# Kernel tuning notes

Hardware: AMD Instinct MI355X
Metric: run time of the kernel (lower is better)

The kernel has to match this reference:

```python
import jax, jax.numpy as jnp
import numpy as np

B, T, V, E, DC, H = 128, 25, 10000, 512, 512, 512
N0 = H + E + DC  # layer-0 concat width
N1 = 2 * H       # layer-1 concat width


def setup_inputs() -> dict:
    key = jax.random.key(0)
    ks = jax.random.split(key, 12)
    def w(k, n):
        return jax.random.normal(k, (n, H), dtype=jnp.float32) / np.float32(np.sqrt(n))
    return {
        "tokens": jax.random.randint(ks[0], (B, T), 0, V),
        "processed_cnn_features": jax.random.normal(ks[1], (B, DC), dtype=jnp.float32),
        "initial_hidden_state": jnp.zeros((2, B, H), dtype=jnp.float32),
        "embedding": jax.random.normal(ks[2], (V, E), dtype=jnp.float32) * 0.1,
        "Wu0": w(ks[3], N0), "Wr0": w(ks[4], N0), "Wc0": w(ks[5], N0),
        "bu0": jnp.zeros((H,), jnp.float32), "br0": jnp.zeros((H,), jnp.float32), "bc0": jnp.zeros((H,), jnp.float32),
        "Wu1": w(ks[6], N1), "Wr1": w(ks[7], N1), "Wc1": w(ks[8], N1),
        "bu1": jnp.zeros((H,), jnp.float32), "br1": jnp.zeros((H,), jnp.float32), "bc1": jnp.zeros((H,), jnp.float32),
        "Wout": jax.random.normal(ks[9], (H, V), dtype=jnp.float32) / np.float32(np.sqrt(H)),
        "bout": jnp.zeros((V,), jnp.float32),
    }


def gru_step(x, h, Wu, bu, Wr, br, Wc, bc):
    xh = jnp.concatenate([x, h], axis=1)
    u = jax.nn.sigmoid(xh @ Wu + bu)
    r = jax.nn.sigmoid(xh @ Wr + br)
    cand = jnp.tanh(jnp.concatenate([x, r * h], axis=1) @ Wc + bc)
    return u * h + (1.0 - u) * cand


def reference(tokens, processed_cnn_features, initial_hidden_state, embedding,
              Wu0, Wr0, Wc0, bu0, br0, bc0,
              Wu1, Wr1, Wc1, bu1, br1, bc1,
              Wout, bout):
    emb = embedding[tokens]              # [B, T, E]
    emb_t = jnp.transpose(emb, (1, 0, 2))  # [T, B, E]

    def step(carry, e_t):
        h0, h1 = carry
        x0 = jnp.concatenate([e_t, processed_cnn_features], axis=1)  # [B, E+DC]
        h0 = gru_step(x0, h0, Wu0, bu0, Wr0, br0, Wc0, bc0)
        h1 = gru_step(h0, h1, Wu1, bu1, Wr1, br1, Wc1, bc1)
        logits = h1 @ Wout + bout  # [B, V]
        return (h0, h1), logits

    (h0, h1), logits_seq = jax.lax.scan(step, (initial_hidden_state[0], initial_hidden_state[1]), emb_t)
    logits = jnp.transpose(logits_seq, (1, 0, 2))  # [B, T, V]
    final_hidden = jnp.stack([h0, h1])             # [2, B, H]
    return logits, final_hidden
```

## Files before the change

### kernel.cpp

```cpp
#include <hip/hip_runtime.h>

#define T_ 25
#define V_ 10000
#define NWG_ 192
#define NGRP_ 8
#define GSZ_ (NWG_ / NGRP_)

typedef short bf16x8 __attribute__((ext_vector_type(8)));
typedef float f32x4 __attribute__((ext_vector_type(4)));

__device__ __forceinline__ short f2bf(float x) {
  union { float f; unsigned u; } v; v.f = x;
  unsigned r = (v.u + 0x7fffu + ((v.u >> 16) & 1u)) >> 16;
  return (short)r;
}
__device__ __forceinline__ float sigm(float z) { return 1.f / (1.f + __expf(-z)); }
__device__ __forceinline__ float tanhfast(float z) {
  float e = __expf(2.f * z);
  return 1.f - 2.f / (e + 1.f);
}

__device__ __forceinline__ void gload_lds16(const void* g, void* l) {
  __builtin_amdgcn_global_load_lds((const __attribute__((address_space(1))) void*)g,
                                   (__attribute__((address_space(3))) void*)l, 16, 0, 0);
}

__device__ __forceinline__ void vwait0() { asm volatile("s_waitcnt vmcnt(0)" ::: "memory"); }
__device__ __forceinline__ void cload16(bf16x8* d, const short* p) {
  asm volatile("global_load_dwordx4 %0, %1, off sc0 sc1" : "=v"(*d) : "v"(p) : "memory");
}
__device__ __forceinline__ void cloadf(float* d, const float* p) {
  asm volatile("global_load_dword %0, %1, off sc0 sc1" : "=v"(*d) : "v"(p) : "memory");
}
__device__ __forceinline__ void cstoref(float* p, float v) {
  asm volatile("global_store_dword %0, %1, off sc0 sc1" :: "v"(p), "v"(v) : "memory");
}
__device__ __forceinline__ void cstores(short* p, int v) {
  asm volatile("global_store_short %0, %1, off sc0 sc1" :: "v"(p), "v"(v) : "memory");
}

__device__ __forceinline__ int FL(int row, int col) {
  return (((col >> 5) * 8 + (row >> 4)) << 9) | (((row & 15) | (((col >> 3) & 3) << 4)) << 3) | (col & 7);
}

__device__ __forceinline__ void gbar(int* bar, int gen) {
  vwait0();
  __syncthreads();
  if (threadIdx.x == 0) {
    const int g = blockIdx.x & (NGRP_ - 1);
    int prev = __hip_atomic_fetch_add(&bar[256 + g * 32], 1, __ATOMIC_RELAXED, __HIP_MEMORY_SCOPE_AGENT);
    if (prev == gen * GSZ_ - 1) {
      int sp = __hip_atomic_fetch_add(&bar[512], 1, __ATOMIC_RELAXED, __HIP_MEMORY_SCOPE_AGENT);
      if (sp == gen * NGRP_ - 1) {
#pragma unroll
        for (int i = 0; i < NGRP_; i++)
          __hip_atomic_store(&bar[i * 32], gen, __ATOMIC_RELAXED, __HIP_MEMORY_SCOPE_AGENT);
      }
    }
    while (__hip_atomic_load(&bar[g * 32], __ATOMIC_RELAXED, __HIP_MEMORY_SCOPE_AGENT) < gen)
      __builtin_amdgcn_s_sleep(1);
  }
  __syncthreads();
}

struct TJob { const float* src; short* dst; int R, C, t0; };
struct TJobs { TJob j[10]; };

__global__ void tcast_all(TJobs J) {
  __shared__ float t[32][33];
  int bid = blockIdx.x;
  int ji = 0;
  while (ji < 9 && bid >= J.j[ji + 1].t0) ji++;
  const float* src = J.j[ji].src;
  short* dst = J.j[ji].dst;
  int R = J.j[ji].R, C = J.j[ji].C;
  int rel = bid - J.j[ji].t0;
  int ctiles = (C + 31) >> 5;
  int rt0 = (rel / ctiles) * 32, ct0 = (rel % ctiles) * 32;
  int tx = threadIdx.x, ty = threadIdx.y;
#pragma unroll
  for (int i = 0; i < 4; i++) {
    int r = rt0 + ty + i * 8, c = ct0 + tx;
    if (r < R && c < C) t[ty + i * 8][tx] = src[(size_t)r * C + c];
  }
  __syncthreads();
#pragma unroll
  for (int i = 0; i < 4; i++) {
    int c = ct0 + ty + i * 8, r = rt0 + tx;
    if (r < R && c < C) dst[(size_t)c * R + r] = f2bf(t[tx][ty + i * 8]);
  }
}

__global__ void build_x0(const int* __restrict__ tok, const float* __restrict__ emb,
                         const float* __restrict__ cnn, short* __restrict__ X0) {
  int row = blockIdx.x;
  int t = row >> 7, b = row & 127;
  int tk = tok[b * T_ + t];
  const float* er = emb + (size_t)tk * 512;
  short* dst = X0 + (size_t)row * 1024;
  for (int i = threadIdx.x; i < 1024; i += 256)
    dst[i] = f2bf(i < 512 ? er[i] : cnn[b * 512 + (i - 512)]);
}

__global__ void init_h(const float* __restrict__ ihs, float* h0f, float* h1f, short* xh1b) {
  int i = blockIdx.x * 256 + threadIdx.x;
  if (i < 65536) {
    int b = i >> 9, h = i & 511;
    float v0 = ihs[i], v1 = ihs[65536 + i];
    h0f[i] = v0; h1f[i] = v1;
    xh1b[FL(b, h)] = f2bf(v0);
    xh1b[FL(b, 512 + h)] = f2bf(v1);
  }
}

__global__ void write_final(const float* __restrict__ h0f, const float* __restrict__ h1f,
                            float* __restrict__ out) {
  int i = blockIdx.x * 256 + threadIdx.x;
  if (i < 65536) {
    out[32000000 + i] = h0f[i];
    out[32000000 + 65536 + i] = h1f[i];
  }
}

struct RP {
  short *xh1b, *rh0b, *xc1b0, *xc1b1, *H1all;
  float *u0f, *u1f, *h0f, *h1f;
  const float *A0;
  const short *Whur0T, *Whc0T, *W1urT, *Wc1T;
  const float *bu1, *br1, *bc1;
  int *bar;
};

template<int NKS>
__device__ __forceinline__ void wload(const short* __restrict__ Wt, int n0, int lane, bf16x8* wfr) {
  const short* p = Wt + (size_t)(n0 + (lane & 15)) * (NKS * 32) + ((lane >> 4) * 8);
#pragma unroll
  for (int ks = 0; ks < NKS; ks++) wfr[ks] = *(const bf16x8*)(p + (size_t)ks * 32);
}

template<int NKS>
__device__ __forceinline__ void kcompute_coh(const short* __restrict__ A, int rb0, int lane,
                                             const bf16x8* __restrict__ wfr, f32x4* acc) {
  const short* ap = A + rb0 * 512 + lane * 8;
  constexpr int NCH = NKS / 4;
  bf16x8 s0[2][4], s1[2][4];
#pragma unroll
  for (int j = 0; j < 4; j++) {
    cload16(&s0[0][j], ap + j * 4096);
    cload16(&s1[0][j], ap + j * 4096 + 512);
  }
#pragma unroll
  for (int c = 0; c < NCH; c++) {
    const int cb = c & 1;
    if (c + 1 < NCH) {
#pragma unroll
      for (int j = 0; j < 4; j++) {
        int ks = (c + 1) * 4 + j;
        cload16(&s0[cb ^ 1][j], ap + ks * 4096);
        cload16(&s1[cb ^ 1][j], ap + ks * 4096 + 512);
      }
      asm volatile("s_waitcnt vmcnt(8)" ::: "memory");
    } else {
      asm volatile("s_waitcnt vmcnt(0)" ::: "memory");
    }
    __builtin_amdgcn_sched_barrier(0);
#pragma unroll
    for (int j = 0; j < 4; j++) {
      int ks = c * 4 + j;
      acc[ks & 1]       = __builtin_amdgcn_mfma_f32_16x16x32_bf16(s0[cb][j], wfr[ks], acc[ks & 1], 0, 0, 0);
      acc[2 + (ks & 1)] = __builtin_amdgcn_mfma_f32_16x16x32_bf16(s1[cb][j], wfr[ks], acc[2 + (ks & 1)], 0, 0, 0);
    }
  }
}

__global__ __launch_bounds__(256) void recurrence(RP p) {
  const int role = blockIdx.x;
  const int tid = threadIdx.x, wv = tid >> 6, lane = tid & 63;
  const int lr = lane & 15, lg = lane >> 4;
  int gen = 0;

  if (role < 64) {
    const int nt = role >> 1, mh = role & 1;
    const int colb = nt * 32 + (wv & 1) * 16;
    const int rb0 = mh * 4 + (wv >> 1) * 2;
    const int col = colb + lr;
    bf16x8 wfr[32]; wload<32>(p.W1urT, colb, lane, wfr);
    gbar(p.bar, ++gen); gbar(p.bar, ++gen);
    for (int t = 0; t < T_; t++) {
      f32x4 acc[4] = {};
      kcompute_coh<32>(p.xh1b, rb0, lane, wfr, acc);
      f32x4 am[2] = { acc[0] + acc[1], acc[2] + acc[3] };
      short* xc = (t & 1) ? p.xc1b1 : p.xc1b0;
      if (colb < 512) {
#pragma unroll
        for (int m = 0; m < 2; m++)
#pragma unroll
          for (int i = 0; i < 4; i++) {
            int row = (rb0 + m) * 16 + lg * 4 + i;
            cstoref(&p.u1f[row * 512 + col], sigm(am[m][i] + p.bu1[col]));
          }
      } else {
        float hv[8];
#pragma unroll
        for (int m = 0; m < 2; m++)
#pragma unroll
          for (int i = 0; i < 4; i++)
            cloadf(&hv[m * 4 + i], &p.h1f[((rb0 + m) * 16 + lg * 4 + i) * 512 + (col - 512)]);
        vwait0(); __builtin_amdgcn_sched_barrier(0);
#pragma unroll
        for (int m = 0; m < 2; m++)
#pragma unroll
          for (int i = 0; i < 4; i++) {
            int row = (rb0 + m) * 16 + lg * 4 + i;
            float s = sigm(am[m][i] + p.br1[col - 512]);
            cstores(&xc[FL(row, col)], f2bf(s * hv[m * 4 + i]));
          }
      }
      gbar(p.bar, ++gen);
      gbar(p.bar, ++gen);
    }
  } else if (role < 128) {
    const int r2 = role - 64;
    const int nt = r2 >> 1, mh = r2 & 1;
    const int colb = nt * 32 + (wv & 1) * 16;
    const int rb0 = mh * 4 + (wv >> 1) * 2;
    const int col = colb + lr;
    bf16x8 wfr[16]; wload<16>(p.Whur0T, colb, lane, wfr);
    auto doP1 = [&](int tt) {
      f32x4 acc[4] = {};
      kcompute_coh<16>(p.xh1b, rb0, lane, wfr, acc);
      f32x4 am[2] = { acc[0] + acc[1], acc[2] + acc[3] };
      const float* a0s = p.A0 + (size_t)tt * 196608;
      if (colb < 512) {
#pragma unroll
        for (int m = 0; m < 2; m++)
#pragma unroll
          for (int i = 0; i < 4; i++) {
            int row = (rb0 + m) * 16 + lg * 4 + i;
            cstoref(&p.u0f[row * 512 + col], sigm(am[m][i] + a0s[row * 1536 + col]));
          }
      } else {
        float hv[8];
#pragma unroll
        for (int m = 0; m < 2; m++)
#pragma unroll
          for (int i = 0; i < 4; i++)
            cloadf(&hv[m * 4 + i], &p.h0f[((rb0 + m) * 16 + lg * 4 + i) * 512 + (col - 512)]);
        vwait0(); __builtin_amdgcn_sched_barrier(0);
#pragma unroll
        for (int m = 0; m < 2; m++)
#pragma unroll
          for (int i = 0; i < 4; i++) {
            int row = (rb0 + m) * 16 + lg * 4 + i;
            float s = sigm(am[m][i] + a0s[row * 1536 + col]);
            cstores(&p.rh0b[FL(row, col - 512)], f2bf(s * hv[m * 4 + i]));
          }
      }
    };
    doP1(0);
    gbar(p.bar, ++gen); gbar(p.bar, ++gen);
    for (int t = 0; t < T_; t++) {
      if (t < T_ - 1) doP1(t + 1);
      gbar(p.bar, ++gen);
      gbar(p.bar, ++gen);
    }
  } else if (role < 160) {
    const int r4 = role - 128;
    const int nt = r4 >> 1, mh = r4 & 1;
    const int colb = nt * 32 + (wv & 1) * 16;
    const int rb0 = mh * 4 + (wv >> 1) * 2;
    const int col = colb + lr;
    bf16x8 wfr[32]; wload<32>(p.Wc1T, colb, lane, wfr);
    gbar(p.bar, ++gen); gbar(p.bar, ++gen);
    for (int t = 0; t < T_; t++) {
      gbar(p.bar, ++gen);
      const short* xc = (t & 1) ? p.xc1b1 : p.xc1b0;
      f32x4 acc[4] = {};
      kcompute_coh<32>(xc, rb0, lane, wfr, acc);
      f32x4 am[2] = { acc[0] + acc[1], acc[2] + acc[3] };
      float uv[8], hv[8];
#pragma unroll
      for (int m = 0; m < 2; m++)
#pragma unroll
        for (int i = 0; i < 4; i++) {
          int row = (rb0 + m) * 16 + lg * 4 + i;
          cloadf(&uv[m * 4 + i], &p.u1f[row * 512 + col]);
          cloadf(&hv[m * 4 + i], &p.h1f[row * 512 + col]);
        }
      vwait0(); __builtin_amdgcn_sched_barrier(0);
#pragma unroll
      for (int m = 0; m < 2; m++)
#pragma unroll
        for (int i = 0; i < 4; i++) {
          int row = (rb0 + m) * 16 + lg * 4 + i;
          float cc = tanhfast(am[m][i] + p.bc1[col]);
          float u = uv[m * 4 + i], h = hv[m * 4 + i];
          float hn = u * h + (1.f - u) * cc;
          cstoref(&p.h1f[row * 512 + col], hn);
          short hb = f2bf(hn);
          cstores(&p.xh1b[FL(row, 512 + col)], hb);
          p.H1all[(size_t)t * 65536 + row * 512 + col] = hb;
        }
      gbar(p.bar, ++gen);
    }
  } else {
    const int r2 = role - 160;
    const int nt = r2 >> 1, mh = r2 & 1;
    const int colb = nt * 32 + (wv & 1) * 16;
    const int rb0 = mh * 4 + (wv >> 1) * 2;
    const int col = colb + lr;
    bf16x8 wfr[16]; wload<16>(p.Whc0T, colb, lane, wfr);
    auto doP2 = [&](int tt) {
      f32x4 acc[4] = {};
      kcompute_coh<16>(p.rh0b, rb0, lane, wfr, acc);
      f32x4 am[2] = { acc[0] + acc[1], acc[2] + acc[3] };
      const float* a0s = p.A0 + (size_t)tt * 196608;
      short* xcw = (tt & 1) ? p.xc1b1 : p.xc1b0;
      float uv[8], hv[8];
#pragma unroll
      for (int m = 0; m < 2; m++)
#pragma unroll
        for (int i = 0; i < 4; i++) {
          int row = (rb0 + m) * 16 + lg * 4 + i;
          cloadf(&uv[m * 4 + i], &p.u0f[row * 512 + col]);
          cloadf(&hv[m * 4 + i], &p.h0f[row * 512 + col]);
        }
      vwait0(); __builtin_amdgcn_sched_barrier(0);
#pragma unroll
      for (int m = 0; m < 2; m++)
#pragma unroll
        for (int i = 0; i < 4; i++) {
          int row = (rb0 + m) * 16 + lg * 4 + i;
          float c = tanhfast(am[m][i] + a0s[row * 1536 + 1024 + col]);
          float u = uv[m * 4 + i], h = hv[m * 4 + i];
          float hn = u * h + (1.f - u) * c;
          cstoref(&p.h0f[row * 512 + col], hn);
          short hb = f2bf(hn);
          cstores(&p.xh1b[FL(row, col)], hb);
          cstores(&xcw[FL(row, col)], hb);
        }
    };
    gbar(p.bar, ++gen);
    doP2(0);
    gbar(p.bar, ++gen);
    for (int t = 0; t < T_; t++) {
      gbar(p.bar, ++gen);
      if (t < T_ - 1) doP2(t + 1);
      gbar(p.bar, ++gen);
    }
  }
}

struct GP {
  const short* A; const short* Bt;
  int lda, ldb, N, K;
  const float* bias0; const float* bias1; const float* bias2;
  float* fdst;
  float* outp; const float* bout;
};

template<int BM, int BN, int VAR>
__device__ __forceinline__ void gemm_core(const GP& p, short* la, short* lb, int bm, int bn, short* smem) {
  const int tid = threadIdx.x;
  const int wave = tid >> 6, lane = tid & 63;
  const int wm = wave >> 1, wn = wave & 1;
  constexpr int WM = BM / 2, WN = BN / 2;
  constexpr int MF = WM / 16, NF = WN / 16;
  const int lr = lane & 15, lg = lane >> 4;
  const short* Abase = p.A + (size_t)bm * BM * p.lda;
  const short* Bbase = p.Bt + (size_t)bn * BN * p.ldb;
  const int bnmax = p.N - bn * BN;
  f32x4 acc[MF][NF] = {};
  const int nkb = p.K >> 6;

  auto stA = [&](int buf, int k0) {
    constexpr int NI = BM / 32;
#pragma unroll
    for (int j = 0; j < NI; j++) {
      int glin = j * 256 + tid;
      int row = glin >> 3, gc = glin & 7;
      int gcs = gc ^ (row & 7);
      gload_lds16(Abase + (size_t)row * p.lda + k0 + gcs * 8,
                  &la[buf * BM * 64 + j * 2048 + wave * 512]);
    }
  };
  auto stB = [&](int buf, int k0) {
    constexpr int NI = BN / 32;
#pragma unroll
    for (int j = 0; j < NI; j++) {
      int glin = j * 256 + tid;
      int row = glin >> 3, gc = glin & 7;
      int gcs = gc ^ (row & 7);
      int rc = row < bnmax ? row : bnmax - 1;
      gload_lds16(Bbase + (size_t)rc * p.ldb + k0 + gcs * 8,
                  &lb[buf * BN * 64 + j * 2048 + wave * 512]);
    }
  };

  stA(0, 0); stB(0, 0);
  __syncthreads();
  int buf = 0;
  for (int kb = 0; kb < nkb; kb++) {
    if (kb + 1 < nkb) { stA(buf ^ 1, (kb + 1) * 64); stB(buf ^ 1, (kb + 1) * 64); }
    bf16x8 af[2][MF], bfr[2][NF];
#pragma unroll
    for (int ks = 0; ks < 2; ks++) {
#pragma unroll
      for (int m = 0; m < MF; m++) {
        int ar = wm * WM + m * 16 + lr;
        af[ks][m] = *(const bf16x8*)&la[buf * BM * 64 + (ar * 8 + ((ks * 4 + lg) ^ (ar & 7))) * 8];
      }
#pragma unroll
      for (int n = 0; n < NF; n++) {
        int br = wn * WN + n * 16 + lr;
        bfr[ks][n] = *(const bf16x8*)&lb[buf * BN * 64 + (br * 8 + ((ks * 4 + lg) ^ (br & 7))) * 8];
      }
    }
#pragma unroll
    for (int ks = 0; ks < 2; ks++)
#pragma unroll
      for (int m = 0; m < MF; m++)
#pragma unroll
        for (int n = 0; n < NF; n++)
          acc[m][n] = __builtin_amdgcn_mfma_f32_16x16x32_bf16(af[ks][m], bfr[ks][n], acc[m][n], 0, 0, 0);
    __syncthreads();
    buf ^= 1;
  }

  if constexpr (VAR == 0) {
#pragma unroll
    for (int m = 0; m < MF; m++)
#pragma unroll
      for (int n = 0; n < NF; n++)
#pragma unroll
        for (int i = 0; i < 4; i++) {
          int row = bm * BM + wm * WM + m * 16 + lg * 4 + i;
          int col = bn * BN + wn * WN + n * 16 + lr;
          if (col >= p.N) continue;
          float bias = col < 512 ? p.bias0[col] : (col < 1024 ? p.bias1[col - 512] : p.bias2[col - 1024]);
          p.fdst[(size_t)row * 1536 + col] = acc[m][n][i] + bias;
        }
  } else {
    float* fs = (float*)smem;
#pragma unroll
    for (int m = 0; m < MF; m++)
#pragma unroll
      for (int n = 0; n < NF; n++)
#pragma unroll
        for (int i = 0; i < 4; i++) {
          int lrow = wm * WM + m * 16 + lg * 4 + i;
          int lcol = wn * WN + n * 16 + lr;
          int col = bn * BN + lcol;
          fs[lrow * 128 + lcol] = acc[m][n][i] + (col < p.N ? p.bout[col] : 0.f);
        }
    __syncthreads();
#pragma unroll
    for (int j = 0; j < 16; j++) {
      int idx = j * 256 + tid;
      int r = idx >> 5, c4 = (idx & 31) << 2;
      int gr = bm * BM + r;
      int tt = gr >> 7, b = gr & 127;
      int col = bn * BN + c4;
      if (col < p.N) {
        f32x4 v = *(const f32x4*)&fs[r * 128 + c4];
        *(f32x4*)&p.outp[((size_t)b * T_ + tt) * V_ + col] = v;
      }
    }
  }
}

template<int BM, int BN, int VAR>
__global__ __launch_bounds__(256) void gemm_one(GP p) {
  __shared__ short smem[2 * BM * 64 + 2 * BN * 64];
  int bm, bn;
  if constexpr (VAR == 5) {
    int lin = blockIdx.y * gridDim.x + blockIdx.x;
    const int nwg = 79 * 25, q = nwg / 8, r8 = nwg % 8;
    int xcd = lin % 8, idx = lin / 8;
    int nlin = (xcd < r8 ? xcd * (q + 1) : r8 * (q + 1) + (xcd - r8) * q) + idx;
    bm = nlin % 25; bn = nlin / 25;
  } else { bm = blockIdx.y; bn = blockIdx.x; }
  gemm_core<BM, BN, VAR>(p, smem, smem + 2 * BM * 64, bm, bn, smem);
}

extern "C" void kernel_launch(void* const* d_in, const int* in_sizes, int n_in,
                              void* d_out, int out_size, void* d_ws, size_t ws_size,
                              hipStream_t stream) {
  const int*   tokens = (const int*)  d_in[0];
  const float* cnn    = (const float*)d_in[1];
  const float* ihs    = (const float*)d_in[2];
  const float* emb    = (const float*)d_in[3];
  const float* Wu0 = (const float*)d_in[4];
  const float* Wr0 = (const float*)d_in[5];
  const float* Wc0 = (const float*)d_in[6];
  const float* bu0 = (const float*)d_in[7];
  const float* br0 = (const float*)d_in[8];
  const float* bc0 = (const float*)d_in[9];
  const float* Wu1 = (const float*)d_in[10];
  const float* Wr1 = (const float*)d_in[11];
  const float* Wc1 = (const float*)d_in[12];
  const float* bu1 = (const float*)d_in[13];
  const float* br1 = (const float*)d_in[14];
  const float* bc1 = (const float*)d_in[15];
  const float* Wout = (const float*)d_in[16];
  const float* bout = (const float*)d_in[17];
  float* out = (float*)d_out;

  char* w = (char*)d_ws;
  size_t off = 0;
  auto alloc = [&](size_t bytes) { void* p = w + off; off += (bytes + 255) & ~255ull; return p; };
  short* WxT    = (short*)alloc(1536 * 1024 * 2);
  short* Whur0T = (short*)alloc(1024 * 512 * 2);
  short* Whc0T  = (short*)alloc(512 * 512 * 2);
  short* W1urT  = (short*)alloc(1024 * 1024 * 2);
  short* Wc1T   = (short*)alloc(512 * 1024 * 2);
  short* WoutT  = (short*)alloc((size_t)10000 * 512 * 2);
  short* X0     = (short*)alloc((size_t)3200 * 1024 * 2);
  float* A0     = (float*)alloc((size_t)3200 * 1536 * 4);
  short* H1all  = (short*)alloc((size_t)3200 * 512 * 2);
  float* u0f    = (float*)alloc(128 * 512 * 4);
  float* u1f    = (float*)alloc(128 * 512 * 4);
  float* h0f    = (float*)alloc(128 * 512 * 4);
  float* h1f    = (float*)alloc(128 * 512 * 4);
  short* rh0b   = (short*)alloc(128 * 512 * 2);
  short* xh1b   = (short*)alloc(128 * 1024 * 2);
  short* xc1b0  = (short*)alloc(128 * 1024 * 2);
  short* xc1b1  = (short*)alloc(128 * 1024 * 2);
  int*   bar    = (int*)alloc(4096);
  (void)ws_size; (void)in_sizes; (void)n_in; (void)out_size;

  {
    TJobs J;
    J.j[0] = { Wu0,              WxT,                1024, 512,  0    };
    J.j[1] = { Wr0,              WxT + 512 * 1024,   1024, 512,  512  };
    J.j[2] = { Wc0,              WxT + 1024 * 1024,  1024, 512,  1024 };
    J.j[3] = { Wu0 + 1024 * 512, Whur0T,             512,  512,  1536 };
    J.j[4] = { Wr0 + 1024 * 512, Whur0T + 512 * 512, 512,  512,  1792 };
    J.j[5] = { Wc0 + 1024 * 512, Whc0T,              512,  512,  2048 };
    J.j[6] = { Wu1,              W1urT,              1024, 512,  2304 };
    J.j[7] = { Wr1,              W1urT + 512 * 1024, 1024, 512,  2816 };
    J.j[8] = { Wc1,              Wc1T,               1024, 512,  3328 };
    J.j[9] = { Wout,             WoutT,              512,  10000, 3840 };
    tcast_all<<<8848, dim3(32, 8), 0, stream>>>(J);
  }

  build_x0<<<3200, 256, 0, stream>>>(tokens, emb, cnn, X0);
  init_h<<<256, 256, 0, stream>>>(ihs, h0f, h1f, xh1b);
  hipMemsetAsync(bar, 0, 4096, stream);

  {
    GP g = {};
    g.A = X0; g.lda = 1024; g.Bt = WxT; g.ldb = 1024; g.N = 1536; g.K = 1024;
    g.bias0 = bu0; g.bias1 = br0; g.bias2 = bc0; g.fdst = A0;
    gemm_one<128, 128, 0><<<dim3(12, 25), 256, 0, stream>>>(g);
  }

  {
    RP r = {};
    r.xh1b = xh1b; r.rh0b = rh0b; r.xc1b0 = xc1b0; r.xc1b1 = xc1b1; r.H1all = H1all;
    r.u0f = u0f; r.u1f = u1f; r.h0f = h0f; r.h1f = h1f;
    r.A0 = A0;
    r.Whur0T = Whur0T; r.Whc0T = Whc0T; r.W1urT = W1urT; r.Wc1T = Wc1T;
    r.bu1 = bu1; r.br1 = br1; r.bc1 = bc1;
    r.bar = bar;
    recurrence<<<dim3(NWG_), 256, 0, stream>>>(r);
  }

  {
    GP g = {};
    g.A = H1all; g.lda = 512; g.Bt = WoutT; g.ldb = 512; g.N = 10000; g.K = 512;
    g.outp = out; g.bout = bout;
    gemm_one<128, 128, 5><<<dim3(79, 25), 256, 0, stream>>>(g);
  }

  write_final<<<256, 256, 0, stream>>>(h0f, h1f, out);
}
```

Baseline: 532.6 us.

## Flatten grid barrier, deepen A-operand prefetch, hoist state loads, fuse final-hidden write

The hierarchical group/super-counter grid barrier becomes a flat scheme over 16 counters. Every block increments its group counter and polls the minimum across all counters, which removes the serial second atomic hop. The coherent A-operand prefetch in the MFMA loop goes from double to triple buffering, and the h/u state loads are issued before the matmul so their latency overlaps it. The final hidden state is now written directly from the recurrence kernel, which drops the separate write_final launch. In exchange, each block issues more polling loads per barrier and uses more registers for the prefetch buffers.

Result: slower. 583.6 us (+9.6%).

```diff
diff --git a/kernel.cpp b/kernel.cpp
--- a/kernel.cpp
+++ b/kernel.cpp
@@ -3,7 +3,7 @@
 #define T_ 25
 #define V_ 10000
 #define NWG_ 192
-#define NGRP_ 8
+#define NGRP_ 16
 #define GSZ_ (NWG_ / NGRP_)
 
 typedef short bf16x8 __attribute__((ext_vector_type(8)));
@@ -26,6 +26,14 @@
 }
 
 __device__ __forceinline__ void vwait0() { asm volatile("s_waitcnt vmcnt(0)" ::: "memory"); }
+__device__ __forceinline__ void vwait_n(int n) {
+  switch (n) {
+    case 0:  asm volatile("s_waitcnt vmcnt(0)"  ::: "memory"); break;
+    case 8:  asm volatile("s_waitcnt vmcnt(8)"  ::: "memory"); break;
+    case 16: asm volatile("s_waitcnt vmcnt(16)" ::: "memory"); break;
+    default: asm volatile("s_waitcnt vmcnt(0)"  ::: "memory"); break;
+  }
+}
 __device__ __forceinline__ void cload16(bf16x8* d, const short* p) {
   asm volatile("global_load_dwordx4 %0, %1, off sc0 sc1" : "=v"(*d) : "v"(p) : "memory");
 }
@@ -47,18 +55,22 @@
   vwait0();
   __syncthreads();
   if (threadIdx.x == 0) {
-    const int g = blockIdx.x & (NGRP_ - 1);
-    int prev = __hip_atomic_fetch_add(&bar[256 + g * 32], 1, __ATOMIC_RELAXED, __HIP_MEMORY_SCOPE_AGENT);
-    if (prev == gen * GSZ_ - 1) {
-      int sp = __hip_atomic_fetch_add(&bar[512], 1, __ATOMIC_RELAXED, __HIP_MEMORY_SCOPE_AGENT);
-      if (sp == gen * NGRP_ - 1) {
-#pragma unroll
-        for (int i = 0; i < NGRP_; i++)
-          __hip_atomic_store(&bar[i * 32], gen, __ATOMIC_RELAXED, __HIP_MEMORY_SCOPE_AGENT);
-      }
-    }
-    while (__hip_atomic_load(&bar[g * 32], __ATOMIC_RELAXED, __HIP_MEMORY_SCOPE_AGENT) < gen)
+    __hip_atomic_fetch_add(&bar[(blockIdx.x & (NGRP_ - 1)) * 32], 1,
+                           __ATOMIC_RELAXED, __HIP_MEMORY_SCOPE_AGENT);
+    const int need = gen * GSZ_;
+    int sweeps = 0;
+    for (;;) {
+      int mn = 0x7fffffff;
+#pragma unroll
+      for (int i = 0; i < NGRP_; i++) {
+        int v = __hip_atomic_load(&bar[i * 32], __ATOMIC_RELAXED, __HIP_MEMORY_SCOPE_AGENT);
+        mn = v < mn ? v : mn;
+      }
+      if (mn >= need) break;
+      if ((++sweeps & 63) == 0)
+        (void)__hip_atomic_load(&bar[0], __ATOMIC_ACQUIRE, __HIP_MEMORY_SCOPE_AGENT);
       __builtin_amdgcn_s_sleep(1);
+    }
   }
   __syncthreads();
 }
@@ -113,21 +125,13 @@
   }
 }
 
-__global__ void write_final(const float* __restrict__ h0f, const float* __restrict__ h1f,
-                            float* __restrict__ out) {
-  int i = blockIdx.x * 256 + threadIdx.x;
-  if (i < 65536) {
-    out[32000000 + i] = h0f[i];
-    out[32000000 + 65536 + i] = h1f[i];
-  }
-}
-
 struct RP {
   short *xh1b, *rh0b, *xc1b0, *xc1b1, *H1all;
   float *u0f, *u1f, *h0f, *h1f;
   const float *A0;
   const short *Whur0T, *Whc0T, *W1urT, *Wc1T;
   const float *bu1, *br1, *bc1;
+  float *outp;
   int *bar;
 };
 
@@ -143,37 +147,38 @@
                                              const bf16x8* __restrict__ wfr, f32x4* acc) {
   const short* ap = A + rb0 * 512 + lane * 8;
   constexpr int NCH = NKS / 4;
-  bf16x8 s0[2][4], s1[2][4];
-#pragma unroll
-  for (int j = 0; j < 4; j++) {
-    cload16(&s0[0][j], ap + j * 4096);
-    cload16(&s1[0][j], ap + j * 4096 + 512);
-  }
+  constexpr int DEPTH = NCH < 3 ? NCH : 3;
+  bf16x8 s0[4][4], s1[4][4];
+#pragma unroll
+  for (int c = 0; c < DEPTH; c++)
+#pragma unroll
+    for (int j = 0; j < 4; j++) {
+      cload16(&s0[c & 3][j], ap + (c * 4 + j) * 4096);
+      cload16(&s1[c & 3][j], ap + (c * 4 + j) * 4096 + 512);
+    }
 #pragma unroll
   for (int c = 0; c < NCH; c++) {
-    const int cb = c & 1;
-    if (c + 1 < NCH) {
-#pragma unroll
-      for (int j = 0; j < 4; j++) {
-        int ks = (c + 1) * 4 + j;
-        cload16(&s0[cb ^ 1][j], ap + ks * 4096);
-        cload16(&s1[cb ^ 1][j], ap + ks * 4096 + 512);
-      }
-      asm volatile("s_waitcnt vmcnt(8)" ::: "memory");
-    } else {
-      asm volatile("s_waitcnt vmcnt(0)" ::: "memory");
-    }
+    const int issued = (DEPTH + c < NCH) ? DEPTH + c : NCH;
+    vwait_n((issued - c - 1) * 8);
     __builtin_amdgcn_sched_barrier(0);
 #pragma unroll
     for (int j = 0; j < 4; j++) {
       int ks = c * 4 + j;
-      acc[ks & 1]       = __builtin_amdgcn_mfma_f32_16x16x32_bf16(s0[cb][j], wfr[ks], acc[ks & 1], 0, 0, 0);
-      acc[2 + (ks & 1)] = __builtin_amdgcn_mfma_f32_16x16x32_bf16(s1[cb][j], wfr[ks], acc[2 + (ks & 1)], 0, 0, 0);
-    }
-  }
-}
-
-__global__ __launch_bounds__(256) void recurrence(RP p) {
+      acc[ks & 1]       = __builtin_amdgcn_mfma_f32_16x16x32_bf16(s0[c & 3][j], wfr[ks], acc[ks & 1], 0, 0, 0);
+      acc[2 + (ks & 1)] = __builtin_amdgcn_mfma_f32_16x16x32_bf16(s1[c & 3][j], wfr[ks], acc[2 + (ks & 1)], 0, 0, 0);
+    }
+    if (DEPTH + c < NCH) {
+      const int nc = DEPTH + c;
+#pragma unroll
+      for (int j = 0; j < 4; j++) {
+        cload16(&s0[nc & 3][j], ap + (nc * 4 + j) * 4096);
+        cload16(&s1[nc & 3][j], ap + (nc * 4 + j) * 4096 + 512);
+      }
+    }
+  }
+}
+
+__global__ __launch_bounds__(256, 1) void recurrence(RP p) {
   const int role = blockIdx.x;
   const int tid = threadIdx.x, wv = tid >> 6, lane = tid & 63;
   const int lr = lane & 15, lg = lane >> 4;
@@ -187,6 +192,14 @@
     bf16x8 wfr[32]; wload<32>(p.W1urT, colb, lane, wfr);
     gbar(p.bar, ++gen); gbar(p.bar, ++gen);
     for (int t = 0; t < T_; t++) {
+      float hv[8];
+      if (colb >= 512) {
+#pragma unroll
+        for (int m = 0; m < 2; m++)
+#pragma unroll
+          for (int i = 0; i < 4; i++)
+            cloadf(&hv[m * 4 + i], &p.h1f[((rb0 + m) * 16 + lg * 4 + i) * 512 + (col - 512)]);
+      }
       f32x4 acc[4] = {};
       kcompute_coh<32>(p.xh1b, rb0, lane, wfr, acc);
       f32x4 am[2] = { acc[0] + acc[1], acc[2] + acc[3] };
@@ -200,13 +213,6 @@
             cstoref(&p.u1f[row * 512 + col], sigm(am[m][i] + p.bu1[col]));
           }
       } else {
-        float hv[8];
-#pragma unroll
-        for (int m = 0; m < 2; m++)
-#pragma unroll
-          for (int i = 0; i < 4; i++)
-            cloadf(&hv[m * 4 + i], &p.h1f[((rb0 + m) * 16 + lg * 4 + i) * 512 + (col - 512)]);
-        vwait0(); __builtin_amdgcn_sched_barrier(0);
 #pragma unroll
         for (int m = 0; m < 2; m++)
 #pragma unroll
@@ -227,6 +233,14 @@
     const int col = colb + lr;
     bf16x8 wfr[16]; wload<16>(p.Whur0T, colb, lane, wfr);
     auto doP1 = [&](int tt) {
+      float hv[8];
+      if (colb >= 512) {
+#pragma unroll
+        for (int m = 0; m < 2; m++)
+#pragma unroll
+          for (int i = 0; i < 4; i++)
+            cloadf(&hv[m * 4 + i], &p.h0f[((rb0 + m) * 16 + lg * 4 + i) * 512 + (col - 512)]);
+      }
       f32x4 acc[4] = {};
       kcompute_coh<16>(p.xh1b, rb0, lane, wfr, acc);
       f32x4 am[2] = { acc[0] + acc[1], acc[2] + acc[3] };
@@ -240,13 +254,6 @@
             cstoref(&p.u0f[row * 512 + col], sigm(am[m][i] + a0s[row * 1536 + col]));
           }
       } else {
-        float hv[8];
-#pragma unroll
-        for (int m = 0; m < 2; m++)
-#pragma unroll
-          for (int i = 0; i < 4; i++)
-            cloadf(&hv[m * 4 + i], &p.h0f[((rb0 + m) * 16 + lg * 4 + i) * 512 + (col - 512)]);
-        vwait0(); __builtin_amdgcn_sched_barrier(0);
 #pragma unroll
         for (int m = 0; m < 2; m++)
 #pragma unroll
@@ -275,9 +282,6 @@
     for (int t = 0; t < T_; t++) {
       gbar(p.bar, ++gen);
       const short* xc = (t & 1) ? p.xc1b1 : p.xc1b0;
-      f32x4 acc[4] = {};
-      kcompute_coh<32>(xc, rb0, lane, wfr, acc);
-      f32x4 am[2] = { acc[0] + acc[1], acc[2] + acc[3] };
       float uv[8], hv[8];
 #pragma unroll
       for (int m = 0; m < 2; m++)
@@ -287,7 +291,9 @@
           cloadf(&uv[m * 4 + i], &p.u1f[row * 512 + col]);
           cloadf(&hv[m * 4 + i], &p.h1f[row * 512 + col]);
         }
-      vwait0(); __builtin_amdgcn_sched_barrier(0);
+      f32x4 acc[4] = {};
+      kcompute_coh<32>(xc, rb0, lane, wfr, acc);
+      f32x4 am[2] = { acc[0] + acc[1], acc[2] + acc[3] };
 #pragma unroll
       for (int m = 0; m < 2; m++)
 #pragma unroll
@@ -300,6 +306,7 @@
           short hb = f2bf(hn);
           cstores(&p.xh1b[FL(row, 512 + col)], hb);
           p.H1all[(size_t)t * 65536 + row * 512 + col] = hb;
+          if (t == T_ - 1) p.outp[32000000 + 65536 + row * 512 + col] = hn;
         }
       gbar(p.bar, ++gen);
     }
@@ -311,21 +318,20 @@
     const int col = colb + lr;
     bf16x8 wfr[16]; wload<16>(p.Whc0T, colb, lane, wfr);
     auto doP2 = [&](int tt) {
+      float uv[8], hv[8];
+#pragma unroll
+      for (int m = 0; m < 2; m++)
+#pragma unroll
+        for (int i = 0; i < 4; i++) {
+          int row = (rb0 + m) * 16 + lg * 4 + i;
+          cloadf(&uv[m * 4 + i], &p.u0f[row * 512 + col]);
+          cloadf(&hv[m * 4 + i], &p.h0f[row * 512 + col]);
+        }
       f32x4 acc[4] = {};
       kcompute_coh<16>(p.rh0b, rb0, lane, wfr, acc);
       f32x4 am[2] = { acc[0] + acc[1], acc[2] + acc[3] };
       const float* a0s = p.A0 + (size_t)tt * 196608;
       short* xcw = (tt & 1) ? p.xc1b1 : p.xc1b0;
-      float uv[8], hv[8];
-#pragma unroll
-      for (int m = 0; m < 2; m++)
-#pragma unroll
-        for (int i = 0; i < 4; i++) {
-          int row = (rb0 + m) * 16 + lg * 4 + i;
-          cloadf(&uv[m * 4 + i], &p.u0f[row * 512 + col]);
-          cloadf(&hv[m * 4 + i], &p.h0f[row * 512 + col]);
-        }
-      vwait0(); __builtin_amdgcn_sched_barrier(0);
 #pragma unroll
       for (int m = 0; m < 2; m++)
 #pragma unroll
@@ -338,6 +344,7 @@
           short hb = f2bf(hn);
           cstores(&p.xh1b[FL(row, col)], hb);
           cstores(&xcw[FL(row, col)], hb);
+          if (tt == T_ - 1) p.outp[32000000 + row * 512 + col] = hn;
         }
     };
     gbar(p.bar, ++gen);
@@ -562,6 +569,7 @@
     r.A0 = A0;
     r.Whur0T = Whur0T; r.Whc0T = Whc0T; r.W1urT = W1urT; r.Wc1T = Wc1T;
     r.bu1 = bu1; r.br1 = br1; r.bc1 = bc1;
+    r.outp = out;
     r.bar = bar;
     recurrence<<<dim3(NWG_), 256, 0, stream>>>(r);
   }
@@ -572,6 +580,4 @@
     g.outp = out; g.bout = bout;
     gemm_one<128, 128, 5><<<dim3(79, 25), 256, 0, stream>>>(g);
   }
-
-  write_final<<<256, 256, 0, stream>>>(h0f, h1f, out);
-}
+}
```
